# Kernel optimization log

Measured on AMD Instinct MI355X. Metric: run time of the kernel, lower is better.

## Reference

```python
import jax, jax.numpy as jnp
from jax import lax
import numpy as np

TOP_K = 2
CAPACITY_FACTOR = 1.0


def setup_inputs() -> dict:
    key = jax.random.key(0)
    kx, kg, k1, k2 = jax.random.split(key, 4)
    B, S, D, F, E = 8, 4096, 512, 1024, 16
    x = jax.random.normal(kx, (B, S, D), dtype=jnp.float32)
    w_gate = jax.random.normal(kg, (D, E), dtype=jnp.float32) * 0.02
    w1 = jax.random.normal(k1, (E, D, 2 * F), dtype=jnp.float32) * 0.02
    w2 = jax.random.normal(k2, (E, F, D), dtype=jnp.float32) * 0.02
    return {"x": x, "w_gate": w_gate, "w1": w1, "w2": w2}


def reference(x, w_gate, w1, w2):
    # Inference mode: no gating noise, dropout is identity.
    B, S, D = x.shape
    E = w_gate.shape[1]
    T = B * S
    capacity = max(1, int(CAPACITY_FACTOR * T / E))  # static

    flat = x.reshape(T, D)
    gate_logits = flat @ w_gate                      # [T, E]
    gate_scores = jax.nn.softmax(gate_logits, axis=-1)
    topk_vals, topk_idx = lax.top_k(gate_scores, TOP_K)  # [T, k]

    phi_mean = gate_scores.mean(axis=0)
    aux_loss = E * jnp.sum(phi_mean * phi_mean)

    # Per-expert combine weight for every token: [E, T]
    onehot = topk_idx[None, :, :] == jnp.arange(E)[:, None, None]  # [E, T, k]
    w_et = jnp.sum(jnp.where(onehot, topk_vals[None], 0.0), axis=-1)  # [E, T]

    # Capacity truncation: keep the `capacity` highest-weight tokens per expert
    sel_w, sel_idx = lax.top_k(w_et, capacity)  # [E, C]; unrouted picks have weight 0

    xs = flat[sel_idx]                                  # [E, C, D] gather
    h = jnp.einsum('ecd,edf->ecf', xs, w1)              # [E, C, 2F]
    h1, h2 = jnp.split(h, 2, axis=-1)
    act = h1 * jax.nn.silu(h2)                          # SwiGLU
    out_e = jnp.einsum('ecf,efd->ecd', act, w2) * sel_w[..., None]  # [E, C, D]

    combined = jnp.zeros((T, D), dtype=flat.dtype).at[sel_idx.reshape(-1)].add(
        out_e.reshape(-1, D))
    return combined.reshape(B, S, D), aux_loss
```

## Files before the change

kernel.cpp:

```cpp
#include <hip/hip_runtime.h>
#include <hip/hip_bf16.h>
#include <math.h>

#define T_TOK 32768
#define D_DIM 512
#define E_EXP 16
#define F_DIM 1024
#define C_CAP 2048

typedef __attribute__((ext_vector_type(8))) __bf16 bf16x8;
typedef __attribute__((ext_vector_type(4))) float f32x4;

__device__ __forceinline__ unsigned short f2bf(float f) {
  unsigned u = __float_as_uint(f);
  u += 0x7FFFu + ((u >> 16) & 1u);
  return (unsigned short)(u >> 16);
}

__device__ __forceinline__ void gld16(const void* gptr, void* ldsptr) {
  __builtin_amdgcn_global_load_lds(
      (__attribute__((address_space(1))) void*)(void*)gptr,
      (__attribute__((address_space(3))) void*)ldsptr, 16, 0, 0);
}

__global__ void transpose_conv_kernel(const float* __restrict__ in,
                                      unsigned short* __restrict__ out,
                                      int R, int Cc) {
  __shared__ float tile[32][33];
  int e = blockIdx.z;
  int r0 = blockIdx.y * 32, c0 = blockIdx.x * 32;
  const float* pin = in + (size_t)e * R * Cc;
  unsigned short* pout = out + (size_t)e * R * Cc;
  int tx = threadIdx.x, ty = threadIdx.y;
  #pragma unroll
  for (int i = 0; i < 32; i += 8)
    tile[ty + i][tx] = pin[(size_t)(r0 + ty + i) * Cc + c0 + tx];
  __syncthreads();
  int t = ty * 32 + tx;
  int oc = t >> 3, og = t & 7;
  ushort4 o;
  o.x = f2bf(tile[og * 4 + 0][oc]);
  o.y = f2bf(tile[og * 4 + 1][oc]);
  o.z = f2bf(tile[og * 4 + 2][oc]);
  o.w = f2bf(tile[og * 4 + 3][oc]);
  *(ushort4*)&pout[(size_t)(c0 + oc) * R + r0 + og * 4] = o;
}

__global__ __launch_bounds__(256) void gate_kernel(
    const float* __restrict__ x, const float* __restrict__ wg,
    float* __restrict__ w_et, float* __restrict__ phi_sum,
    unsigned short* __restrict__ xb) {
  __shared__ float wgl[D_DIM * E_EXP];
  __shared__ float phil[E_EXP];
  int tid = threadIdx.x;
  for (int i = tid; i < D_DIM * E_EXP; i += 256) wgl[i] = wg[i];
  if (tid < E_EXP) phil[tid] = 0.f;
  __syncthreads();

  int g = tid >> 4;
  int e = tid & 15;
  int t = blockIdx.x * 16 + g;

  float acc = 0.f;
  const float* xr = x + (size_t)t * D_DIM;
  #pragma unroll 4
  for (int d = 0; d < D_DIM; d += 4) {
    float4 xv = *(const float4*)(xr + d);
    acc = fmaf(xv.x, wgl[(d + 0) * 16 + e], acc);
    acc = fmaf(xv.y, wgl[(d + 1) * 16 + e], acc);
    acc = fmaf(xv.z, wgl[(d + 2) * 16 + e], acc);
    acc = fmaf(xv.w, wgl[(d + 3) * 16 + e], acc);
  }

  unsigned short* xrow = xb + (size_t)t * D_DIM;
  #pragma unroll
  for (int j = 0; j < 8; ++j) {
    int idx = j * 16 + e;
    float4 v = *(const float4*)(xr + idx * 4);
    ushort4 o;
    o.x = f2bf(v.x); o.y = f2bf(v.y); o.z = f2bf(v.z); o.w = f2bf(v.w);
    ((ushort4*)xrow)[idx] = o;
  }

  float m = acc;
  for (int off = 8; off; off >>= 1) m = fmaxf(m, __shfl_xor(m, off));
  float p = expf(acc - m);
  float s = p;
  for (int off = 8; off; off >>= 1) s += __shfl_xor(s, off);
  float score = p / s;
  atomicAdd(&phil[e], score);

  float v1 = score; int i1 = e;
  for (int off = 8; off; off >>= 1) {
    float ov = __shfl_xor(v1, off); int oi = __shfl_xor(i1, off);
    if (ov > v1 || (ov == v1 && oi < i1)) { v1 = ov; i1 = oi; }
  }
  float sc2 = (e == i1) ? -1.f : score;
  float v2 = sc2; int i2 = e;
  for (int off = 8; off; off >>= 1) {
    float ov = __shfl_xor(v2, off); int oi = __shfl_xor(i2, off);
    if (ov > v2 || (ov == v2 && oi < i2)) { v2 = ov; i2 = oi; }
  }
  if (e == 0) {
    w_et[(size_t)i1 * T_TOK + t] = v1;
    w_et[(size_t)i2 * T_TOK + t] = v2;
  }
  __syncthreads();
  if (tid < E_EXP) atomicAdd(&phi_sum[tid], phil[tid]);
}

__global__ void aux_kernel(const float* __restrict__ phi_sum, float* __restrict__ out_aux) {
  if (threadIdx.x == 0) {
    float s = 0.f;
    for (int e = 0; e < E_EXP; ++e) {
      float pm = phi_sum[e] / (float)T_TOK;
      s += pm * pm;
    }
    *out_aux = (float)E_EXP * s;
  }
}

template<int P>
__global__ __launch_bounds__(256) void s_hist(
    const float* __restrict__ w_et, unsigned* __restrict__ hist,
    unsigned* __restrict__ prefix, unsigned* __restrict__ krem,
    unsigned* __restrict__ done, unsigned* __restrict__ arrive) {
  int c = blockIdx.x, e = blockIdx.y, tid = threadIdx.x;
  if (P > 0 && done[e]) return;
  __shared__ unsigned lh[2048];
  for (int i = tid; i < 2048; i += 256) lh[i] = 0;
  __syncthreads();
  const float* w = w_et + (size_t)e * T_TOK + c * 2048;
  unsigned pfx = (P > 0) ? prefix[e] : 0u;
  #pragma unroll
  for (int i = 0; i < 8; ++i) {
    unsigned b = __float_as_uint(w[i * 256 + tid]);
    if (P == 0) { if (b) atomicAdd(&lh[b >> 21], 1u); }
    else if (P == 1) { if ((b >> 21) == (pfx >> 21)) atomicAdd(&lh[(b >> 10) & 0x7FFu], 1u); }
    else { if ((b >> 10) == (pfx >> 10)) atomicAdd(&lh[b & 0x3FFu], 1u); }
  }
  __syncthreads();
  for (int i = tid; i < 2048; i += 256)
    if (lh[i]) atomicAdd(&hist[e * 2048 + i], lh[i]);

  __threadfence();
  __shared__ unsigned s_last;
  if (tid == 0) s_last = (atomicAdd(&arrive[P * 16 + e], 1u) == 15u) ? 1u : 0u;
  __syncthreads();
  if (!s_last) return;
  __threadfence();
  if (tid >= 64) return;
  int lane = tid;
  const int BPL = (P == 2) ? 16 : 32;
  const int SH = (P == 0) ? 21 : (P == 1) ? 10 : 0;
  const unsigned* h = hist + e * 2048;
  unsigned S = 0;
  for (int i = 0; i < BPL; ++i) S += h[lane * BPL + i];
  unsigned U = S;
  #pragma unroll
  for (int off = 1; off < 64; off <<= 1) {
    unsigned t2 = __shfl_down(U, off);
    if (lane + off < 64) U += t2;
  }
  unsigned Unext = __shfl_down(U, 1);
  if (lane == 63) Unext = 0;
  unsigned k = (P == 0) ? (unsigned)C_CAP : krem[e];
  if (P == 0 && lane == 0) {
    if (U < k) { done[e] = 1; prefix[e] = 0; krem[e] = 0; }
    else done[e] = 0;
  }
  if (U >= k && Unext < k) {
    unsigned cum = Unext; int chosen = 0; unsigned knew = 0;
    for (int i = BPL - 1; i >= 0; --i) {
      unsigned hh = h[lane * BPL + i];
      if (cum + hh >= k) { chosen = lane * BPL + i; knew = k - cum; break; }
      cum += hh;
    }
    if (P == 0) prefix[e] = ((unsigned)chosen) << SH;
    else prefix[e] = prefix[e] | (((unsigned)chosen) << SH);
    krem[e] = knew;
  }
}

__global__ __launch_bounds__(256) void s_count(
    const float* __restrict__ w_et, const unsigned* __restrict__ prefix,
    unsigned* __restrict__ cnt) {
  int c = blockIdx.x, e = blockIdx.y, tid = threadIdx.x;
  unsigned thr = prefix[e];
  const uint4* up = (const uint4*)(w_et + (size_t)e * T_TOK + c * 2048 + tid * 8);
  uint4 va = up[0], vb = up[1];
  unsigned gt = 0, eq = 0;
  unsigned vals[8] = {va.x, va.y, va.z, va.w, vb.x, vb.y, vb.z, vb.w};
  #pragma unroll
  for (int i = 0; i < 8; ++i) {
    if (vals[i] > thr) gt++;
    else if (vals[i] == thr) eq++;
  }
  __shared__ unsigned sc[256];
  sc[tid] = (gt << 16) | eq;
  __syncthreads();
  for (int s = 128; s; s >>= 1) {
    if (tid < s) sc[tid] += sc[tid + s];
    __syncthreads();
  }
  if (tid == 0) cnt[e * 16 + c] = sc[0];
}

__global__ __launch_bounds__(256) void s_write(
    const float* __restrict__ w_et, const unsigned* __restrict__ prefix,
    const unsigned* __restrict__ cnt,
    int* __restrict__ sel_idx, float* __restrict__ sel_w,
    int* __restrict__ tokmap, unsigned* __restrict__ cnt_tok) {
  int c = blockIdx.x, e = blockIdx.y, tid = threadIdx.x;
  unsigned thr = prefix[e];
  __shared__ unsigned s_gb, s_eb, s_gt, s_eq;
  if (tid == 0) {
    unsigned g = 0, q = 0, gb = 0, eb = 0;
    #pragma unroll
    for (int c2 = 0; c2 < 16; ++c2) {
      unsigned p = cnt[e * 16 + c2];
      if (c2 < c) { gb += p >> 16; eb += p & 0xFFFFu; }
      g += p >> 16; q += p & 0xFFFFu;
    }
    s_gb = gb; s_eb = eb; s_gt = g; s_eq = (unsigned)C_CAP - g;
  }
  const uint4* up = (const uint4*)(w_et + (size_t)e * T_TOK + c * 2048 + tid * 8);
  uint4 va = up[0], vb = up[1];
  unsigned vals[8] = {va.x, va.y, va.z, va.w, vb.x, vb.y, vb.z, vb.w};
  unsigned gt = 0, eq = 0;
  #pragma unroll
  for (int i = 0; i < 8; ++i) {
    if (vals[i] > thr) gt++;
    else if (vals[i] == thr) eq++;
  }
  __shared__ unsigned sc[256];
  unsigned mine = (gt << 16) | eq;
  sc[tid] = mine;
  __syncthreads();
  for (int off = 1; off < 256; off <<= 1) {
    unsigned add = (tid >= off) ? sc[tid - off] : 0u;
    __syncthreads();
    sc[tid] += add;
    __syncthreads();
  }
  unsigned excl = sc[tid] - mine;
  unsigned gpos = s_gb + (excl >> 16);
  unsigned qpos = s_eb + (excl & 0xFFFFu);
  unsigned gtotal = s_gt, eqtake = s_eq;
  int* si = sel_idx + (size_t)e * C_CAP;
  float* sw = sel_w + (size_t)e * C_CAP;
  int tokbase = c * 2048 + tid * 8;
  #pragma unroll
  for (int i = 0; i < 8; ++i) {
    unsigned b = vals[i];
    int tok = tokbase + i;
    if (b > thr) {
      si[gpos] = tok; sw[gpos] = __uint_as_float(b);
      unsigned j = atomicAdd(&cnt_tok[tok], 1u);
      tokmap[tok * 2 + j] = e * C_CAP + (int)gpos;
      gpos++;
    } else if (b == thr && qpos < eqtake) {
      si[gtotal + qpos] = tok; sw[gtotal + qpos] = __uint_as_float(b);
      if (b != 0u) {
        unsigned j = atomicAdd(&cnt_tok[tok], 1u);
        tokmap[tok * 2 + j] = e * C_CAP + (int)(gtotal + qpos);
      }
      qpos++;
    }
  }
}


#define PIPE_BARRIER() do { __builtin_amdgcn_s_barrier(); __builtin_amdgcn_sched_barrier(0); } while (0)

__global__ __launch_bounds__(256, 3) void gemm1_kernel(
    const unsigned short* __restrict__ xb,
    const unsigned short* __restrict__ w1t,
    const int* __restrict__ sel_idx,
    unsigned short* __restrict__ act) {
  __shared__ __align__(16) unsigned short As[3 * 4096];
  __shared__ __align__(16) unsigned short Bs[3 * 4096];
  int bid = (blockIdx.x & 7) * 512 + (blockIdx.x >> 3);
  int nt = bid & 15, mt = (bid >> 4) & 15, e = bid >> 8;
  int tid = threadIdx.x, lane = tid & 63, wid = tid >> 6;
  int wr = wid >> 1, wc = wid & 1;
  int cl = lane & 15, rg = lane >> 4;

  int c0 = tid, c1 = 256 + tid;
  int r0 = c0 >> 2, gk0 = (c0 & 3) ^ ((r0 >> 1) & 3);
  int r1 = c1 >> 2, gk1 = (c1 & 3) ^ ((r1 >> 1) & 3);
  int tok0 = sel_idx[e * C_CAP + mt * 128 + r0];
  int tok1 = sel_idx[e * C_CAP + mt * 128 + r1];
  const unsigned short* ag0 = xb + (size_t)tok0 * D_DIM + gk0 * 8;
  const unsigned short* ag1 = xb + (size_t)tok1 * D_DIM + gk1 * 8;
  int hcol0 = (r0 < 64) ? (nt * 64 + r0) : (F_DIM + nt * 64 + (r0 - 64));
  int hcol1 = (r1 < 64) ? (nt * 64 + r1) : (F_DIM + nt * 64 + (r1 - 64));
  const unsigned short* bg0 = w1t + ((size_t)e * 2 * F_DIM + hcol0) * D_DIM + gk0 * 8;
  const unsigned short* bg1 = w1t + ((size_t)e * 2 * F_DIM + hcol1) * D_DIM + gk1 * 8;
  char* Ab = (char*)As;
  char* Bb = (char*)Bs;

#define G1_STAGE(buf, kt) do { \
    gld16(ag0 + (kt) * 32, Ab + (buf) * 8192 + tid * 16); \
    gld16(ag1 + (kt) * 32, Ab + (buf) * 8192 + 4096 + tid * 16); \
    gld16(bg0 + (kt) * 32, Bb + (buf) * 8192 + tid * 16); \
    gld16(bg1 + (kt) * 32, Bb + (buf) * 8192 + 4096 + tid * 16); \
  } while (0)

  f32x4 zero = {0.f, 0.f, 0.f, 0.f};
  f32x4 acc[4][4];
  #pragma unroll
  for (int m = 0; m < 4; ++m)
    #pragma unroll
    for (int n = 0; n < 4; ++n) acc[m][n] = zero;

#define G1_COMPUTE(buf) do { \
    const unsigned short* Ap = As + (buf) * 4096; \
    const unsigned short* Bp = Bs + (buf) * 4096; \
    bf16x8 av[4], bv[4]; \
    _Pragma("unroll") \
    for (int m = 0; m < 4; ++m) { \
      int ra = wr * 64 + m * 16 + cl; \
      av[m] = *(const bf16x8*)&Ap[(ra * 4 + (rg ^ ((ra >> 1) & 3))) * 8]; \
    } \
    _Pragma("unroll") \
    for (int n = 0; n < 4; ++n) { \
      int rb = ((n < 2) ? (wc * 32 + n * 16) : (64 + wc * 32 + (n - 2) * 16)) + cl; \
      bv[n] = *(const bf16x8*)&Bp[(rb * 4 + (rg ^ ((rb >> 1) & 3))) * 8]; \
    } \
    _Pragma("unroll") \
    for (int m = 0; m < 4; ++m) \
      _Pragma("unroll") \
      for (int n = 0; n < 4; ++n) \
        acc[m][n] = __builtin_amdgcn_mfma_f32_16x16x32_bf16(av[m], bv[n], acc[m][n], 0, 0, 0); \
  } while (0)

  const int NK = D_DIM / 32;
  G1_STAGE(0, 0);
  G1_STAGE(1, 1);
  int bc = 0, bs = 2;
  for (int kt = 0; kt < NK - 1; ++kt) {
    asm volatile("s_waitcnt vmcnt(4)" ::: "memory");
    PIPE_BARRIER();
    if (kt + 2 < NK) { G1_STAGE(bs, kt + 2); bs = (bs == 2) ? 0 : bs + 1; }
    __builtin_amdgcn_sched_barrier(0);
    G1_COMPUTE(bc);
    bc = (bc == 2) ? 0 : bc + 1;
  }
  asm volatile("s_waitcnt vmcnt(0)" ::: "memory");
  PIPE_BARRIER();
  G1_COMPUTE(bc);

  #pragma unroll
  for (int m = 0; m < 4; ++m) {
    #pragma unroll
    for (int n = 0; n < 2; ++n) {
      #pragma unroll
      for (int r = 0; r < 4; ++r) {
        int row = mt * 128 + wr * 64 + m * 16 + rg * 4 + r;
        int col = nt * 64 + wc * 32 + n * 16 + cl;
        float h1 = acc[m][n][r];
        float h2 = acc[m][n + 2][r];
        float sg = h2 / (1.f + __expf(-h2));
        act[((size_t)e * C_CAP + row) * F_DIM + col] = f2bf(h1 * sg);
      }
    }
  }
#undef G1_STAGE
#undef G1_COMPUTE
}

__global__ __launch_bounds__(256, 3) void gemm2_kernel(
    const unsigned short* __restrict__ act,
    const unsigned short* __restrict__ w2t,
    const float* __restrict__ sel_w,
    float* __restrict__ outE) {
  __shared__ __align__(16) unsigned short As[3 * 4096];
  __shared__ __align__(16) unsigned short Bs[3 * 4096];
  int bid = (blockIdx.x & 7) * 128 + (blockIdx.x >> 3);
  int nt = bid & 3, mt = (bid >> 2) & 15, e = bid >> 6;
  int tid = threadIdx.x, lane = tid & 63, wid = tid >> 6;
  int wr = wid >> 1, wc = wid & 1;
  int cl = lane & 15, rg = lane >> 4;

  int c0 = tid, c1 = 256 + tid;
  int r0 = c0 >> 2, gk0 = (c0 & 3) ^ ((r0 >> 1) & 3);
  int r1 = c1 >> 2, gk1 = (c1 & 3) ^ ((r1 >> 1) & 3);
  const unsigned short* ag0 = act + ((size_t)e * C_CAP + mt * 128 + r0) * F_DIM + gk0 * 8;
  const unsigned short* ag1 = act + ((size_t)e * C_CAP + mt * 128 + r1) * F_DIM + gk1 * 8;
  const unsigned short* bg0 = w2t + ((size_t)e * D_DIM + nt * 128 + r0) * F_DIM + gk0 * 8;
  const unsigned short* bg1 = w2t + ((size_t)e * D_DIM + nt * 128 + r1) * F_DIM + gk1 * 8;
  char* Ab = (char*)As;
  char* Bb = (char*)Bs;

#define G2_STAGE(buf, kt) do { \
    gld16(ag0 + (kt) * 32, Ab + (buf) * 8192 + tid * 16); \
    gld16(ag1 + (kt) * 32, Ab + (buf) * 8192 + 4096 + tid * 16); \
    gld16(bg0 + (kt) * 32, Bb + (buf) * 8192 + tid * 16); \
    gld16(bg1 + (kt) * 32, Bb + (buf) * 8192 + 4096 + tid * 16); \
  } while (0)

  f32x4 zero = {0.f, 0.f, 0.f, 0.f};
  f32x4 acc[4][4];
  #pragma unroll
  for (int m = 0; m < 4; ++m)
    #pragma unroll
    for (int n = 0; n < 4; ++n) acc[m][n] = zero;

#define G2_COMPUTE(buf) do { \
    const unsigned short* Ap = As + (buf) * 4096; \
    const unsigned short* Bp = Bs + (buf) * 4096; \
    bf16x8 av[4], bv[4]; \
    _Pragma("unroll") \
    for (int m = 0; m < 4; ++m) { \
      int ra = wr * 64 + m * 16 + cl; \
      av[m] = *(const bf16x8*)&Ap[(ra * 4 + (rg ^ ((ra >> 1) & 3))) * 8]; \
    } \
    _Pragma("unroll") \
    for (int n = 0; n < 4; ++n) { \
      int rb = wc * 64 + n * 16 + cl; \
      bv[n] = *(const bf16x8*)&Bp[(rb * 4 + (rg ^ ((rb >> 1) & 3))) * 8]; \
    } \
    _Pragma("unroll") \
    for (int m = 0; m < 4; ++m) \
      _Pragma("unroll") \
      for (int n = 0; n < 4; ++n) \
        acc[m][n] = __builtin_amdgcn_mfma_f32_16x16x32_bf16(av[m], bv[n], acc[m][n], 0, 0, 0); \
  } while (0)

  const int NK = F_DIM / 32;
  G2_STAGE(0, 0);
  G2_STAGE(1, 1);
  int bc = 0, bs = 2;
  for (int kt = 0; kt < NK - 1; ++kt) {
    asm volatile("s_waitcnt vmcnt(4)" ::: "memory");
    PIPE_BARRIER();
    if (kt + 2 < NK) { G2_STAGE(bs, kt + 2); bs = (bs == 2) ? 0 : bs + 1; }
    __builtin_amdgcn_sched_barrier(0);
    G2_COMPUTE(bc);
    bc = (bc == 2) ? 0 : bc + 1;
  }
  asm volatile("s_waitcnt vmcnt(0)" ::: "memory");
  PIPE_BARRIER();
  G2_COMPUTE(bc);

  #pragma unroll
  for (int m = 0; m < 4; ++m) {
    #pragma unroll
    for (int r = 0; r < 4; ++r) {
      int slot = mt * 128 + wr * 64 + m * 16 + rg * 4 + r;
      float wgt = sel_w[e * C_CAP + slot];
      float* orow = outE + ((size_t)e * C_CAP + slot) * D_DIM;
      #pragma unroll
      for (int n = 0; n < 4; ++n) {
        int col = nt * 128 + wc * 64 + n * 16 + cl;
        orow[col] = acc[m][n][r] * wgt;
      }
    }
  }
#undef G2_STAGE
#undef G2_COMPUTE
}

__global__ __launch_bounds__(256) void combine_kernel(
    const float* __restrict__ outE, const int* __restrict__ tokmap,
    const unsigned* __restrict__ cnt_tok, float* __restrict__ out) {
  int t = blockIdx.x * 4 + (threadIdx.x >> 6);
  int lane = threadIdx.x & 63;
  unsigned cnt = cnt_tok[t];
  float4 a0 = {0.f, 0.f, 0.f, 0.f}, a1 = {0.f, 0.f, 0.f, 0.f};
  for (unsigned j = 0; j < cnt; ++j) {
    int s = tokmap[t * 2 + j];
    const float4* p = (const float4*)(outE + (size_t)s * D_DIM);
    float4 v0 = p[lane], v1 = p[lane + 64];
    a0.x += v0.x; a0.y += v0.y; a0.z += v0.z; a0.w += v0.w;
    a1.x += v1.x; a1.y += v1.y; a1.z += v1.z; a1.w += v1.w;
  }
  float4* o = (float4*)(out + (size_t)t * D_DIM);
  o[lane] = a0;
  o[lane + 64] = a1;
}

extern "C" void kernel_launch(void* const* d_in, const int* in_sizes, int n_in,
                              void* d_out, int out_size, void* d_ws, size_t ws_size,
                              hipStream_t stream) {
  const float* x  = (const float*)d_in[0];
  const float* wg = (const float*)d_in[1];
  const float* w1 = (const float*)d_in[2];
  const float* w2 = (const float*)d_in[3];
  float* out = (float*)d_out;

  char* ws = (char*)d_ws;
  size_t off = 0;
  auto carve = [&](size_t bytes) -> void* {
    void* p = ws + off;
    off += (bytes + 255) & ~(size_t)255;
    return p;
  };
  float* w_et            = (float*)carve((size_t)E_EXP * T_TOK * 4);
  float* phi             = (float*)carve(64);
  int* sel_i             = (int*)carve((size_t)E_EXP * C_CAP * 4);
  float* sel_wv          = (float*)carve((size_t)E_EXP * C_CAP * 4);
  unsigned short* xb     = (unsigned short*)carve((size_t)T_TOK * D_DIM * 2);
  unsigned short* w1t    = (unsigned short*)carve((size_t)E_EXP * 2 * F_DIM * D_DIM * 2);
  unsigned short* w2t    = (unsigned short*)carve((size_t)E_EXP * D_DIM * F_DIM * 2);
  unsigned short* actb   = (unsigned short*)carve((size_t)E_EXP * C_CAP * F_DIM * 2);
  unsigned* hist0        = (unsigned*)carve((size_t)E_EXP * 2048 * 4);
  unsigned* hist1        = (unsigned*)carve((size_t)E_EXP * 2048 * 4);
  unsigned* hist2        = (unsigned*)carve((size_t)E_EXP * 2048 * 4);
  unsigned* prefix       = (unsigned*)carve(64 * 4);
  unsigned* krem         = (unsigned*)carve(64 * 4);
  unsigned* done         = (unsigned*)carve(64 * 4);
  unsigned* cnt          = (unsigned*)carve(256 * 4);
  unsigned* arrive       = (unsigned*)carve(64 * 4);
  int* tokmap            = (int*)carve((size_t)T_TOK * 2 * 4);
  unsigned* cnt_tok      = (unsigned*)carve((size_t)T_TOK * 4);
  if (off > ws_size) return;

  float* outE = (float*)xb;

  hipMemsetAsync(w_et, 0, (size_t)E_EXP * T_TOK * 4, stream);
  hipMemsetAsync(phi, 0, 64, stream);
  hipMemsetAsync(hist0, 0, (size_t)E_EXP * 2048 * 4 * 3, stream);
  hipMemsetAsync(arrive, 0, 64 * 4, stream);
  hipMemsetAsync(cnt_tok, 0, (size_t)T_TOK * 4, stream);

  transpose_conv_kernel<<<dim3(2 * F_DIM / 32, D_DIM / 32, E_EXP), dim3(32, 8), 0, stream>>>(
      w1, w1t, D_DIM, 2 * F_DIM);
  transpose_conv_kernel<<<dim3(D_DIM / 32, F_DIM / 32, E_EXP), dim3(32, 8), 0, stream>>>(
      w2, w2t, F_DIM, D_DIM);
  gate_kernel<<<T_TOK / 16, 256, 0, stream>>>(x, wg, w_et, phi, xb);

  s_hist<0><<<dim3(16, 16), 256, 0, stream>>>(w_et, hist0, prefix, krem, done, arrive);
  s_hist<1><<<dim3(16, 16), 256, 0, stream>>>(w_et, hist1, prefix, krem, done, arrive);
  s_hist<2><<<dim3(16, 16), 256, 0, stream>>>(w_et, hist2, prefix, krem, done, arrive);
  s_count<<<dim3(16, 16), 256, 0, stream>>>(w_et, prefix, cnt);
  s_write<<<dim3(16, 16), 256, 0, stream>>>(w_et, prefix, cnt, sel_i, sel_wv,
                                            tokmap, cnt_tok);

  aux_kernel<<<1, 64, 0, stream>>>(phi, out + (size_t)T_TOK * D_DIM);
  gemm1_kernel<<<E_EXP * 16 * 16, 256, 0, stream>>>(xb, w1t, sel_i, actb);
  gemm2_kernel<<<E_EXP * 16 * 4, 256, 0, stream>>>(actb, w2t, sel_wv, outE);
  combine_kernel<<<T_TOK / 4, 256, 0, stream>>>(outE, tokmap, cnt_tok, out);
}
```

Baseline: 347.3 us.

## Fuse combine into gemm2 via atomic scatter-add and merge setup launches

Removes the separate combine kernel and its token map: gemm2 now atomically adds weighted expert outputs straight into the zeroed output rows selected by sel_idx. The gate kernel writes every expert's w_et entry itself, so the large w_et memset goes away. The two weight-transpose launches become one, and the small memsets are merged into one contiguous zeroing. The cost is a full output memset plus float atomics in the gemm2 epilogue, which adds contention and makes the summation order nondeterministic.

After: 365.0 us. 5.1% more time.

```diff
diff --git a/kernel.cpp b/kernel.cpp
--- a/kernel.cpp
+++ b/kernel.cpp
@@ -23,12 +23,17 @@
       (__attribute__((address_space(3))) void*)ldsptr, 16, 0, 0);
 }
 
-__global__ void transpose_conv_kernel(const float* __restrict__ in,
-                                      unsigned short* __restrict__ out,
-                                      int R, int Cc) {
+__global__ void transpose_conv2_kernel(const float* __restrict__ w1,
+                                       const float* __restrict__ w2,
+                                       unsigned short* __restrict__ w1t,
+                                       unsigned short* __restrict__ w2t) {
   __shared__ float tile[32][33];
-  int e = blockIdx.z;
-  int r0 = blockIdx.y * 32, c0 = blockIdx.x * 32;
+  int e = blockIdx.y;
+  int b = blockIdx.x;
+  const float* in; unsigned short* out; int R, Cc, bx, by;
+  if (b < 1024) { in = w1; out = w1t; R = D_DIM; Cc = 2 * F_DIM; bx = b & 63; by = b >> 6; }
+  else { b -= 1024; in = w2; out = w2t; R = F_DIM; Cc = D_DIM; bx = b & 15; by = b >> 4; }
+  int r0 = by * 32, c0 = bx * 32;
   const float* pin = in + (size_t)e * R * Cc;
   unsigned short* pout = out + (size_t)e * R * Cc;
   int tx = threadIdx.x, ty = threadIdx.y;
@@ -101,10 +106,8 @@
     float ov = __shfl_xor(v2, off); int oi = __shfl_xor(i2, off);
     if (ov > v2 || (ov == v2 && oi < i2)) { v2 = ov; i2 = oi; }
   }
-  if (e == 0) {
-    w_et[(size_t)i1 * T_TOK + t] = v1;
-    w_et[(size_t)i2 * T_TOK + t] = v2;
-  }
+  float val = (e == i1) ? v1 : ((e == i2) ? v2 : 0.f);
+  w_et[(size_t)e * T_TOK + t] = val;
   __syncthreads();
   if (tid < E_EXP) atomicAdd(&phi_sum[tid], phil[tid]);
 }
@@ -209,8 +212,7 @@
 __global__ __launch_bounds__(256) void s_write(
     const float* __restrict__ w_et, const unsigned* __restrict__ prefix,
     const unsigned* __restrict__ cnt,
-    int* __restrict__ sel_idx, float* __restrict__ sel_w,
-    int* __restrict__ tokmap, unsigned* __restrict__ cnt_tok) {
+    int* __restrict__ sel_idx, float* __restrict__ sel_w) {
   int c = blockIdx.x, e = blockIdx.y, tid = threadIdx.x;
   unsigned thr = prefix[e];
   __shared__ unsigned s_gb, s_eb, s_gt, s_eq;
@@ -253,19 +255,10 @@
   #pragma unroll
   for (int i = 0; i < 8; ++i) {
     unsigned b = vals[i];
-    int tok = tokbase + i;
     if (b > thr) {
-      si[gpos] = tok; sw[gpos] = __uint_as_float(b);
-      unsigned j = atomicAdd(&cnt_tok[tok], 1u);
-      tokmap[tok * 2 + j] = e * C_CAP + (int)gpos;
-      gpos++;
+      si[gpos] = tokbase + i; sw[gpos] = __uint_as_float(b); gpos++;
     } else if (b == thr && qpos < eqtake) {
-      si[gtotal + qpos] = tok; sw[gtotal + qpos] = __uint_as_float(b);
-      if (b != 0u) {
-        unsigned j = atomicAdd(&cnt_tok[tok], 1u);
-        tokmap[tok * 2 + j] = e * C_CAP + (int)(gtotal + qpos);
-      }
-      qpos++;
+      si[gtotal + qpos] = tokbase + i; sw[gtotal + qpos] = __uint_as_float(b); qpos++;
     }
   }
 }
@@ -373,8 +366,9 @@
 __global__ __launch_bounds__(256, 3) void gemm2_kernel(
     const unsigned short* __restrict__ act,
     const unsigned short* __restrict__ w2t,
+    const int* __restrict__ sel_idx,
     const float* __restrict__ sel_w,
-    float* __restrict__ outE) {
+    float* __restrict__ out) {
   __shared__ __align__(16) unsigned short As[3 * 4096];
   __shared__ __align__(16) unsigned short Bs[3 * 4096];
   int bid = (blockIdx.x & 7) * 128 + (blockIdx.x >> 3);
@@ -450,35 +444,17 @@
     for (int r = 0; r < 4; ++r) {
       int slot = mt * 128 + wr * 64 + m * 16 + rg * 4 + r;
       float wgt = sel_w[e * C_CAP + slot];
-      float* orow = outE + ((size_t)e * C_CAP + slot) * D_DIM;
+      int tok = sel_idx[e * C_CAP + slot];
+      float* orow = out + (size_t)tok * D_DIM;
       #pragma unroll
       for (int n = 0; n < 4; ++n) {
         int col = nt * 128 + wc * 64 + n * 16 + cl;
-        orow[col] = acc[m][n][r] * wgt;
+        atomicAdd(&orow[col], acc[m][n][r] * wgt);
       }
     }
   }
 #undef G2_STAGE
 #undef G2_COMPUTE
-}
-
-__global__ __launch_bounds__(256) void combine_kernel(
-    const float* __restrict__ outE, const int* __restrict__ tokmap,
-    const unsigned* __restrict__ cnt_tok, float* __restrict__ out) {
-  int t = blockIdx.x * 4 + (threadIdx.x >> 6);
-  int lane = threadIdx.x & 63;
-  unsigned cnt = cnt_tok[t];
-  float4 a0 = {0.f, 0.f, 0.f, 0.f}, a1 = {0.f, 0.f, 0.f, 0.f};
-  for (unsigned j = 0; j < cnt; ++j) {
-    int s = tokmap[t * 2 + j];
-    const float4* p = (const float4*)(outE + (size_t)s * D_DIM);
-    float4 v0 = p[lane], v1 = p[lane + 64];
-    a0.x += v0.x; a0.y += v0.y; a0.z += v0.z; a0.w += v0.w;
-    a1.x += v1.x; a1.y += v1.y; a1.z += v1.z; a1.w += v1.w;
-  }
-  float4* o = (float4*)(out + (size_t)t * D_DIM);
-  o[lane] = a0;
-  o[lane + 64] = a1;
 }
 
 extern "C" void kernel_launch(void* const* d_in, const int* in_sizes, int n_in,
@@ -498,48 +474,37 @@
     return p;
   };
   float* w_et            = (float*)carve((size_t)E_EXP * T_TOK * 4);
-  float* phi             = (float*)carve(64);
   int* sel_i             = (int*)carve((size_t)E_EXP * C_CAP * 4);
   float* sel_wv          = (float*)carve((size_t)E_EXP * C_CAP * 4);
   unsigned short* xb     = (unsigned short*)carve((size_t)T_TOK * D_DIM * 2);
   unsigned short* w1t    = (unsigned short*)carve((size_t)E_EXP * 2 * F_DIM * D_DIM * 2);
   unsigned short* w2t    = (unsigned short*)carve((size_t)E_EXP * D_DIM * F_DIM * 2);
   unsigned short* actb   = (unsigned short*)carve((size_t)E_EXP * C_CAP * F_DIM * 2);
+  float* phi             = (float*)carve(256);
   unsigned* hist0        = (unsigned*)carve((size_t)E_EXP * 2048 * 4);
   unsigned* hist1        = (unsigned*)carve((size_t)E_EXP * 2048 * 4);
   unsigned* hist2        = (unsigned*)carve((size_t)E_EXP * 2048 * 4);
-  unsigned* prefix       = (unsigned*)carve(64 * 4);
-  unsigned* krem         = (unsigned*)carve(64 * 4);
-  unsigned* done         = (unsigned*)carve(64 * 4);
-  unsigned* cnt          = (unsigned*)carve(256 * 4);
-  unsigned* arrive       = (unsigned*)carve(64 * 4);
-  int* tokmap            = (int*)carve((size_t)T_TOK * 2 * 4);
-  unsigned* cnt_tok      = (unsigned*)carve((size_t)T_TOK * 4);
+  unsigned* prefix       = (unsigned*)carve(256);
+  unsigned* krem         = (unsigned*)carve(256);
+  unsigned* done         = (unsigned*)carve(256);
+  unsigned* cnt          = (unsigned*)carve(1024);
+  unsigned* arrive       = (unsigned*)carve(256);
+  size_t zero_bytes = (size_t)((char*)(arrive + 64) - (char*)phi);
   if (off > ws_size) return;
 
-  float* outE = (float*)xb;
-
-  hipMemsetAsync(w_et, 0, (size_t)E_EXP * T_TOK * 4, stream);
-  hipMemsetAsync(phi, 0, 64, stream);
-  hipMemsetAsync(hist0, 0, (size_t)E_EXP * 2048 * 4 * 3, stream);
-  hipMemsetAsync(arrive, 0, 64 * 4, stream);
-  hipMemsetAsync(cnt_tok, 0, (size_t)T_TOK * 4, stream);
-
-  transpose_conv_kernel<<<dim3(2 * F_DIM / 32, D_DIM / 32, E_EXP), dim3(32, 8), 0, stream>>>(
-      w1, w1t, D_DIM, 2 * F_DIM);
-  transpose_conv_kernel<<<dim3(D_DIM / 32, F_DIM / 32, E_EXP), dim3(32, 8), 0, stream>>>(
-      w2, w2t, F_DIM, D_DIM);
+  hipMemsetAsync(phi, 0, zero_bytes, stream);
+  hipMemsetAsync(d_out, 0, (size_t)out_size * 4, stream);
+
+  transpose_conv2_kernel<<<dim3(1536, 16), dim3(32, 8), 0, stream>>>(w1, w2, w1t, w2t);
   gate_kernel<<<T_TOK / 16, 256, 0, stream>>>(x, wg, w_et, phi, xb);
 
   s_hist<0><<<dim3(16, 16), 256, 0, stream>>>(w_et, hist0, prefix, krem, done, arrive);
   s_hist<1><<<dim3(16, 16), 256, 0, stream>>>(w_et, hist1, prefix, krem, done, arrive);
   s_hist<2><<<dim3(16, 16), 256, 0, stream>>>(w_et, hist2, prefix, krem, done, arrive);
   s_count<<<dim3(16, 16), 256, 0, stream>>>(w_et, prefix, cnt);
-  s_write<<<dim3(16, 16), 256, 0, stream>>>(w_et, prefix, cnt, sel_i, sel_wv,
-                                            tokmap, cnt_tok);
+  s_write<<<dim3(16, 16), 256, 0, stream>>>(w_et, prefix, cnt, sel_i, sel_wv);
 
   aux_kernel<<<1, 64, 0, stream>>>(phi, out + (size_t)T_TOK * D_DIM);
   gemm1_kernel<<<E_EXP * 16 * 16, 256, 0, stream>>>(xb, w1t, sel_i, actb);
-  gemm2_kernel<<<E_EXP * 16 * 4, 256, 0, stream>>>(actb, w2t, sel_wv, outE);
-  combine_kernel<<<T_TOK / 4, 256, 0, stream>>>(outE, tokmap, cnt_tok, out);
-}
+  gemm2_kernel<<<E_EXP * 16 * 4, 256, 0, stream>>>(actb, w2t, sel_i, sel_wv, out);
+}
```
